# Performance work log

Hardware: AMD Instinct MI355X
Metric: run time of the kernel (lower is better)

Reference implementation:

```python
import jax, jax.numpy as jnp
import numpy as np

DIM = 512
NUM_GROUPS = 32
HEADS = 16
HEAD_DIM = 32
EPS = 1e-6


def group_norm(x, w, b, num_groups=NUM_GROUPS, eps=EPS):
    # x: [B, C, H, W]
    B, C, H, W = x.shape
    xg = x.reshape(B, num_groups, -1)
    mean = xg.mean(axis=-1, keepdims=True)
    var = xg.var(axis=-1, keepdims=True)
    xg = (xg - mean) / jnp.sqrt(var + eps)
    x = xg.reshape(B, C, H, W)
    return x * w[None, :, None, None] + b[None, :, None, None]


def conv1x1(x, w, b):
    # x: [B, C, H, W], w: [O, C], b: [O]
    return jnp.einsum('bchw,oc->bohw', x, w) + b[None, :, None, None]


def setup_inputs() -> dict:
    key = jax.random.key(0)
    ks = jax.random.split(key, 12)
    s = 1.0 / np.sqrt(DIM)
    d = {
        'x': jax.random.normal(ks[0], (1, DIM, 64, 64), dtype=jnp.float32),
        'gn_w': jnp.ones((DIM,), dtype=jnp.float32),
        'gn_b': jnp.zeros((DIM,), dtype=jnp.float32),
        'wq': jax.random.normal(ks[1], (DIM, DIM), dtype=jnp.float32) * s,
        'bq': jax.random.normal(ks[2], (DIM,), dtype=jnp.float32) * 0.01,
        'wk': jax.random.normal(ks[3], (DIM, DIM), dtype=jnp.float32) * s,
        'bk': jax.random.normal(ks[4], (DIM,), dtype=jnp.float32) * 0.01,
        'wv': jax.random.normal(ks[5], (DIM, DIM), dtype=jnp.float32) * s,
        'bv': jax.random.normal(ks[6], (DIM,), dtype=jnp.float32) * 0.01,
        'wo': jax.random.normal(ks[7], (DIM, DIM), dtype=jnp.float32) * s,
        'bo': jax.random.normal(ks[8], (DIM,), dtype=jnp.float32) * 0.01,
    }
    return d


def reference(x, gn_w, gn_b, wq, bq, wk, bk, wv, bv, wo, bo):
    B, C, H, W = x.shape
    N = H * W
    scale = HEAD_DIM ** -0.5

    q_in = x
    qn = group_norm(x, gn_w, gn_b)
    # Faithful to source: v-branch applies norm_q to the already-normalized q.
    vn = group_norm(qn, gn_w, gn_b)

    q = conv1x1(qn, wq, bq)
    k = conv1x1(vn, wk, bk)
    v = conv1x1(vn, wv, bv)

    def to_tokens(t):
        # [B, C, H, W] -> [B, heads, N, head_dim]
        return t.reshape(B, HEADS, HEAD_DIM, N).transpose(0, 1, 3, 2)

    q, k, v = to_tokens(q), to_tokens(k), to_tokens(v)

    attn = jax.nn.softmax(jnp.einsum('bhnd,bhmd->bhnm', q, k) * scale, axis=-1)
    out = jnp.einsum('bhnm,bhmd->bhnd', attn, v)  # [B, heads, N, head_dim]
    out = out.transpose(0, 1, 3, 2).reshape(B, C, H, W)
    out = conv1x1(out, wo, bo)
    return (out + q_in) / jnp.sqrt(jnp.float32(2.0))
```

## Files before the change

kernel.cpp:

```cpp
#include <hip/hip_runtime.h>

#define NTOK 4096
#define CHAN 512
#define GSIZE 65536
#define RSQRT2 0.7071067811865476f
#define SCALE 0.17677669529663687f
#define WB_OFF 32768
#define QT_OFF (WB_OFF + 2097152)
#define WS_NEEDED ((size_t)(QT_OFF + 4194304))

typedef unsigned short ushort_t;
typedef __attribute__((ext_vector_type(8))) short bf16x8;
typedef __attribute__((ext_vector_type(8))) _Float16 f16x8;
typedef __attribute__((ext_vector_type(4))) float f32x4;

__device__ __forceinline__ ushort_t f2b(float f) {
    unsigned u = __float_as_uint(f);
    unsigned r = (u + 0x7FFFu + ((u >> 16) & 1u)) >> 16;
    return (ushort_t)r;
}
__device__ __forceinline__ unsigned pack2r(float a, float b) {
    unsigned ua = __float_as_uint(a), ub = __float_as_uint(b);
    return ((ua + 0x8000u) >> 16) | ((ub + 0x8000u) & 0xFFFF0000u);
}
__device__ __forceinline__ unsigned packh2(float a, float b) {
    return __builtin_bit_cast(unsigned, __builtin_amdgcn_cvt_pkrtz(a, b));
}
__device__ __forceinline__ ushort_t f2h(float f) {
    return (ushort_t)(packh2(f, f) & 0xFFFFu);
}
__device__ __forceinline__ bf16x8 ldfrag(const ushort_t* p) {
    return __builtin_bit_cast(bf16x8, *(const uint4*)p);
}
__device__ __forceinline__ f16x8 ldfragh(const ushort_t* p) {
    return __builtin_bit_cast(f16x8, *(const uint4*)p);
}
__device__ __forceinline__ void ldg2lds16(const void* g, void* l) {
    __builtin_amdgcn_global_load_lds(
        (const __attribute__((address_space(1))) void*)g,
        (__attribute__((address_space(3))) void*)l, 16, 0, 0);
}

__global__ void diag_kernel(float* out, float v) {
    if (threadIdx.x == 0 && blockIdx.x == 0) out[0] = v;
}

__global__ __launch_bounds__(256) void gn_sums(const float* __restrict__ x,
                                               float* __restrict__ S,
                                               float* __restrict__ SS) {
    int c = blockIdx.x, t = threadIdx.x;
    const float4* p = (const float4*)(x + (size_t)c * 4096);
    float s = 0.f, ss = 0.f;
    #pragma unroll
    for (int i = 0; i < 4; i++) {
        float4 f = p[i * 256 + t];
        s += f.x + f.y + f.z + f.w;
        ss += f.x * f.x + f.y * f.y + f.z * f.z + f.w * f.w;
    }
    #pragma unroll
    for (int off = 32; off > 0; off >>= 1) {
        s += __shfl_xor(s, off);
        ss += __shfl_xor(ss, off);
    }
    __shared__ float as[4], bs[4];
    int w = t >> 6;
    if ((t & 63) == 0) { as[w] = s; bs[w] = ss; }
    __syncthreads();
    if (t == 0) {
        S[c] = as[0] + as[1] + as[2] + as[3];
        SS[c] = bs[0] + bs[1] + bs[2] + bs[3];
    }
}

__global__ __launch_bounds__(512) void gn_coef(const float* __restrict__ S,
                                               const float* __restrict__ SS,
                                               const float* __restrict__ gnw,
                                               const float* __restrict__ gnb,
                                               float* __restrict__ qa,
                                               float* __restrict__ qd,
                                               float* __restrict__ va,
                                               float* __restrict__ vd) {
    int c = threadIdx.x;
    float Sc = S[c], SSc = SS[c];
    float gs = Sc, gss = SSc;
    #pragma unroll
    for (int off = 1; off < 16; off <<= 1) {
        gs += __shfl_xor(gs, off);
        gss += __shfl_xor(gss, off);
    }
    float mu = gs * (1.f / GSIZE);
    float var = gss * (1.f / GSIZE) - mu * mu;
    float r1 = rsqrtf(var + 1e-6f);
    float wc = gnw[c], bc = gnb[c];
    float a1 = r1 * wc;
    float d1 = bc - mu * a1;
    qa[c] = a1; qd[c] = d1;
    float S2 = a1 * Sc + 4096.f * d1;
    float SS2 = a1 * a1 * SSc + 2.f * a1 * d1 * Sc + 4096.f * d1 * d1;
    float gs2 = S2, gss2 = SS2;
    #pragma unroll
    for (int off = 1; off < 16; off <<= 1) {
        gs2 += __shfl_xor(gs2, off);
        gss2 += __shfl_xor(gss2, off);
    }
    float mu2 = gs2 * (1.f / GSIZE);
    float var2 = gss2 * (1.f / GSIZE) - mu2 * mu2;
    float r2 = rsqrtf(var2 + 1e-6f);
    float a2 = r2 * wc;
    va[c] = a1 * a2;
    vd[c] = a2 * (d1 - mu2) + bc;
}

__global__ __launch_bounds__(256) void bias_fold(const float* __restrict__ wq,
                                                 const float* __restrict__ wk,
                                                 const float* __restrict__ wv,
                                                 const float* __restrict__ bq,
                                                 const float* __restrict__ bk,
                                                 const float* __restrict__ bv,
                                                 const float* __restrict__ qd,
                                                 const float* __restrict__ vd,
                                                 float* __restrict__ bqf,
                                                 float* __restrict__ bkf,
                                                 float* __restrict__ bvf) {
    int row = blockIdx.x * 4 + (threadIdx.x >> 6);
    int lane = threadIdx.x & 63;
    int m = row >> 9;
    int o = row & 511;
    const float* W = (m == 0) ? wq : (m == 1) ? wk : wv;
    const float* b = (m == 0) ? bq : (m == 1) ? bk : bv;
    const float* d = (m == 0) ? qd : vd;
    float* outp    = (m == 0) ? bqf : (m == 1) ? bkf : bvf;
    const float4* wr = (const float4*)(W + (size_t)o * 512) + lane * 2;
    const float4* dr = (const float4*)d + lane * 2;
    float4 a0 = wr[0], a1 = wr[1], d0 = dr[0], d1 = dr[1];
    float acc = a0.x * d0.x + a0.y * d0.y + a0.z * d0.z + a0.w * d0.w
              + a1.x * d1.x + a1.y * d1.y + a1.z * d1.z + a1.w * d1.w;
    #pragma unroll
    for (int off = 32; off > 0; off >>= 1) acc += __shfl_xor(acc, off);
    if (lane == 0) outp[o] = b[o] + acc;
}

__global__ __launch_bounds__(256) void wprep(const float* __restrict__ wq,
                                             const float* __restrict__ wk,
                                             const float* __restrict__ wv,
                                             const float* __restrict__ wo,
                                             const float* __restrict__ qa,
                                             const float* __restrict__ va,
                                             ushort_t* __restrict__ Wb) {
    int y = blockIdx.y;
    const float* src = (y == 0) ? wq : (y == 1) ? wk : (y == 2) ? wv : wo;
    int i = (blockIdx.x * 256 + threadIdx.x) * 4;
    float4 f = *(const float4*)(src + i);
    if (y < 3) {
        const float* aff = (y == 0) ? qa : va;
        float4 a = *(const float4*)(aff + (i & 511));
        f.x *= a.x; f.y *= a.y; f.z *= a.z; f.w *= a.w;
    }
    uint2 u;
    u.x = pack2r(f.x, f.y);
    u.y = pack2r(f.z, f.w);
    *(uint2*)(Wb + (size_t)y * 262144 + i) = u;
}

__global__ __launch_bounds__(256) void qkv_mfma(const float* __restrict__ x,
                                                const ushort_t* __restrict__ Wb,
                                                const float* __restrict__ bqf,
                                                const float* __restrict__ bkf,
                                                const float* __restrict__ bvf,
                                                ushort_t* __restrict__ QT,
                                                ushort_t* __restrict__ KT,
                                                ushort_t* __restrict__ Vb) {
    __shared__ __align__(16) ushort_t Wl[128][72];
    __shared__ __align__(16) ushort_t Bn[64][72];
    __shared__ __align__(16) ushort_t Tl[64][136];
    int t = threadIdx.x;
    int nbase = blockIdx.x << 6;
    int y = blockIdx.y;
    int buf = y >> 2;
    int obase = (y & 3) << 7;
    const ushort_t* Wsrc = Wb + (size_t)buf * 262144;
    const float* bias = (buf == 0) ? bqf : (buf == 1) ? bkf : bvf;

    int w = t >> 6, lane = t & 63, q15 = lane & 15, quad = lane >> 4;
    f32x4 acc[2][4];
    #pragma unroll
    for (int i = 0; i < 2; i++)
        #pragma unroll
        for (int j = 0; j < 4; j++) acc[i][j] = (f32x4){0.f, 0.f, 0.f, 0.f};

    int tok = t & 63, c8 = t >> 6;
    for (int ck = 0; ck < 512; ck += 64) {
        __syncthreads();
        #pragma unroll
        for (int i = 0; i < 4; i++) {
            int idx = 4 * t + i;
            int row = idx >> 3, seg = idx & 7;
            *(uint4*)&Wl[row][seg * 8] =
                *(const uint4*)&Wsrc[(size_t)(obase + row) * 512 + ck + seg * 8];
        }
        {
            float v[16];
            #pragma unroll
            for (int i = 0; i < 16; i++)
                v[i] = x[(size_t)(ck + c8 * 16 + i) * NTOK + nbase + tok];
            uint4 u0, u1;
            u0.x = pack2r(v[0], v[1]);   u0.y = pack2r(v[2], v[3]);
            u0.z = pack2r(v[4], v[5]);   u0.w = pack2r(v[6], v[7]);
            u1.x = pack2r(v[8], v[9]);   u1.y = pack2r(v[10], v[11]);
            u1.z = pack2r(v[12], v[13]); u1.w = pack2r(v[14], v[15]);
            *(uint4*)&Bn[tok][c8 * 16] = u0;
            *(uint4*)&Bn[tok][c8 * 16 + 8] = u1;
        }
        __syncthreads();
        #pragma unroll
        for (int kk = 0; kk < 2; kk++) {
            bf16x8 af0 = ldfrag(&Wl[w * 32 + q15][kk * 32 + quad * 8]);
            bf16x8 af1 = ldfrag(&Wl[w * 32 + 16 + q15][kk * 32 + quad * 8]);
            #pragma unroll
            for (int n8 = 0; n8 < 4; n8++) {
                bf16x8 bfv = ldfrag(&Bn[n8 * 16 + q15][kk * 32 + quad * 8]);
                acc[0][n8] = __builtin_amdgcn_mfma_f32_16x16x32_bf16(af0, bfv, acc[0][n8], 0, 0, 0);
                acc[1][n8] = __builtin_amdgcn_mfma_f32_16x16x32_bf16(af1, bfv, acc[1][n8], 0, 0, 0);
            }
        }
    }

    if (buf == 2) {
        #pragma unroll
        for (int mi = 0; mi < 2; mi++)
            #pragma unroll
            for (int r = 0; r < 4; r++) {
                int o = obase + w * 32 + mi * 16 + quad * 4 + r;
                float bo = bias[o];
                #pragma unroll
                for (int n8 = 0; n8 < 4; n8++)
                    Vb[(size_t)o * NTOK + nbase + n8 * 16 + q15] = f2h(acc[mi][n8][r] + bo);
            }
        return;
    }

    ushort_t* dstT = (buf == 0) ? QT : KT;
    float qs = (buf == 0) ? SCALE : 1.0f;
    __syncthreads();
    #pragma unroll
    for (int mi = 0; mi < 2; mi++)
        #pragma unroll
        for (int r = 0; r < 4; r++) {
            int mloc = w * 32 + mi * 16 + quad * 4 + r;
            float bo = bias[obase + mloc];
            #pragma unroll
            for (int n8 = 0; n8 < 4; n8++)
                Tl[n8 * 16 + q15][mloc] = f2b((acc[mi][n8][r] + bo) * qs);
        }
    __syncthreads();
    #pragma unroll
    for (int i = 0; i < 4; i++) {
        int idx = 4 * t + i;
        int row = idx >> 4, ch = idx & 15;
        uint4 u = *(const uint4*)&Tl[row][ch * 8];
        *(uint4*)&dstT[(size_t)(nbase + row) * 512 + obase + ch * 8] = u;
    }
}

__global__ __launch_bounds__(512, 4) void attn_v13(ushort_t* __restrict__ QT,
                                                   const ushort_t* __restrict__ KT,
                                                   const ushort_t* __restrict__ V) {
    __shared__ __align__(16) ushort_t KtF[2][8192];
    __shared__ __align__(16) ushort_t VtF[2][8192];
    int h = blockIdx.y;
    int t = threadIdx.x;
    int w = t >> 6, lane = t & 63, q15 = lane & 15, quad = lane >> 4;
    int qbase = (blockIdx.x << 7) + w * 16;
    int hc = h * 32;
    const ushort_t* Vh = V + (size_t)hc * NTOK;

    bf16x8 qf = ldfrag(&QT[(size_t)(qbase + q15) * 512 + hc + quad * 8]);

    const uint4 onesu = {0x3C003C00u, 0x3C003C00u, 0x3C003C00u, 0x3C003C00u};
    const f16x8 ones = __builtin_bit_cast(f16x8, onesu);

    f32x4 o[2] = {{0.f, 0.f, 0.f, 0.f}, {0.f, 0.f, 0.f, 0.f}};
    f32x4 lacc = {0.f, 0.f, 0.f, 0.f};

    auto issue = [&](int j0, int b) {
        #pragma unroll
        for (int i = 0; i < 2; i++) {
            int sbase = (w << 6) + (i << 9);
            int idx = sbase + lane;
            int krow = idx >> 2;
            int gd = (idx & 3) ^ ((krow >> 1) & 3);
            int rp = krow & 63;
            int srcr = (krow & 192) | (rp & 0x23) | ((rp & 0x0C) << 1) | ((rp & 0x10) >> 2);
            ldg2lds16(&KT[(size_t)(j0 + srcr) * 512 + hc + gd * 8],
                      &KtF[b][sbase * 8]);
        }
        #pragma unroll
        for (int i = 0; i < 2; i++) {
            int sbase = (w << 6) + (i << 9);
            int idx = sbase + lane;
            int d = idx >> 5;
            int gd = (idx & 31) ^ (d & 7);
            ldg2lds16(&Vh[(size_t)d * NTOK + j0 + gd * 8],
                      &VtF[b][sbase * 8]);
        }
    };

    issue(0, 0);
    int ksp8 = (quad ^ ((q15 >> 1) & 3)) * 8;
    int vq = q15 & 7;

    for (int tt = 0; tt < 16; tt++) {
        int cur = tt & 1;
        __syncthreads();
        if (tt < 15) issue((tt + 1) << 8, cur ^ 1);
        const ushort_t* KtC = KtF[cur];
        const ushort_t* VtC = VtF[cur];

        #pragma unroll
        for (int h2 = 0; h2 < 4; h2++) {
            f32x4 st[4];
            __builtin_amdgcn_s_setprio(1);
            #pragma unroll
            for (int kt = 0; kt < 4; kt++) {
                bf16x8 kf = ldfrag(&KtC[(h2 * 64 + kt * 16 + q15) * 32 + ksp8]);
                f32x4 z = {0.f, 0.f, 0.f, 0.f};
                st[kt] = __builtin_amdgcn_mfma_f32_16x16x32_bf16(kf, qf, z, 0, 0, 0);
            }
            __builtin_amdgcn_s_setprio(0);

            #pragma unroll
            for (int kt = 0; kt < 4; kt++)
                #pragma unroll
                for (int r = 0; r < 4; r++)
                    st[kt][r] = __expf(st[kt][r]);

            int g0 = ((h2 * 8 + quad) ^ vq) * 8;
            int g1 = g0 ^ 32;
            f16x8 v00 = ldfragh(&VtC[q15 * 256 + g0]);
            f16x8 v01 = ldfragh(&VtC[(16 + q15) * 256 + g0]);
            f16x8 v10 = ldfragh(&VtC[q15 * 256 + g1]);
            f16x8 v11 = ldfragh(&VtC[(16 + q15) * 256 + g1]);

            uint4 p0u, p1u;
            p0u.x = packh2(st[0][0], st[0][1]);
            p0u.y = packh2(st[0][2], st[0][3]);
            p0u.z = packh2(st[1][0], st[1][1]);
            p0u.w = packh2(st[1][2], st[1][3]);
            p1u.x = packh2(st[2][0], st[2][1]);
            p1u.y = packh2(st[2][2], st[2][3]);
            p1u.z = packh2(st[3][0], st[3][1]);
            p1u.w = packh2(st[3][2], st[3][3]);
            f16x8 pf0 = __builtin_bit_cast(f16x8, p0u);
            f16x8 pf1 = __builtin_bit_cast(f16x8, p1u);
            __builtin_amdgcn_s_setprio(1);
            o[0] = __builtin_amdgcn_mfma_f32_16x16x32_f16(pf0, v00, o[0], 0, 0, 0);
            o[1] = __builtin_amdgcn_mfma_f32_16x16x32_f16(pf0, v01, o[1], 0, 0, 0);
            lacc = __builtin_amdgcn_mfma_f32_16x16x32_f16(pf0, ones, lacc, 0, 0, 0);
            o[0] = __builtin_amdgcn_mfma_f32_16x16x32_f16(pf1, v10, o[0], 0, 0, 0);
            o[1] = __builtin_amdgcn_mfma_f32_16x16x32_f16(pf1, v11, o[1], 0, 0, 0);
            lacc = __builtin_amdgcn_mfma_f32_16x16x32_f16(pf1, ones, lacc, 0, 0, 0);
            __builtin_amdgcn_s_setprio(0);
        }
    }

    #pragma unroll
    for (int r = 0; r < 4; r++) {
        float li = 1.f / lacc[r];
        int q = quad * 4 + r;
        QT[(size_t)(qbase + q) * 512 + hc + q15]      = f2b(o[0][r] * li);
        QT[(size_t)(qbase + q) * 512 + hc + 16 + q15] = f2b(o[1][r] * li);
    }
}

__global__ __launch_bounds__(256) void oproj_mfma(const ushort_t* __restrict__ OT,
                                                  const ushort_t* __restrict__ Wob,
                                                  const float* __restrict__ bo,
                                                  const float* __restrict__ x,
                                                  float* __restrict__ out) {
    __shared__ __align__(16) ushort_t Wl[64][40];
    __shared__ __align__(16) ushort_t Bn[64][40];
    int t = threadIdx.x;
    int nbase = blockIdx.x << 6;
    int obase = blockIdx.y << 6;
    int w = t >> 6, lane = t & 63, q15 = lane & 15, quad = lane >> 4;

    f32x4 acc[4];
    #pragma unroll
    for (int i = 0; i < 4; i++) acc[i] = (f32x4){0.f, 0.f, 0.f, 0.f};

    int arow = t >> 2, aseg = t & 3;
    for (int ck = 0; ck < 512; ck += 32) {
        __syncthreads();
        *(uint4*)&Wl[arow][aseg * 8] =
            *(const uint4*)&Wob[(size_t)(obase + arow) * 512 + ck + aseg * 8];
        *(uint4*)&Bn[arow][aseg * 8] =
            *(const uint4*)&OT[(size_t)(nbase + arow) * 512 + ck + aseg * 8];
        __syncthreads();
        bf16x8 af = ldfrag(&Wl[w * 16 + q15][quad * 8]);
        #pragma unroll
        for (int n8 = 0; n8 < 4; n8++) {
            bf16x8 bfv = ldfrag(&Bn[n8 * 16 + q15][quad * 8]);
            acc[n8] = __builtin_amdgcn_mfma_f32_16x16x32_bf16(af, bfv, acc[n8], 0, 0, 0);
        }
    }

    #pragma unroll
    for (int r = 0; r < 4; r++) {
        int o = obase + w * 16 + quad * 4 + r;
        float b = bo[o];
        #pragma unroll
        for (int n8 = 0; n8 < 4; n8++) {
            size_t idx = (size_t)o * NTOK + nbase + n8 * 16 + q15;
            out[idx] = (acc[n8][r] + b + x[idx]) * RSQRT2;
        }
    }
}

extern "C" void kernel_launch(void* const* d_in, const int* in_sizes, int n_in,
                              void* d_out, int out_size, void* d_ws, size_t ws_size,
                              hipStream_t stream) {
    const float* x   = (const float*)d_in[0];
    const float* gnw = (const float*)d_in[1];
    const float* gnb = (const float*)d_in[2];
    const float* wq  = (const float*)d_in[3];
    const float* bq  = (const float*)d_in[4];
    const float* wk  = (const float*)d_in[5];
    const float* bk  = (const float*)d_in[6];
    const float* wv  = (const float*)d_in[7];
    const float* bv  = (const float*)d_in[8];
    const float* wo  = (const float*)d_in[9];
    const float* bo  = (const float*)d_in[10];
    float* out = (float*)d_out;

    if (ws_size < WS_NEEDED) {
        diag_kernel<<<1, 64, 0, stream>>>(out, (float)(ws_size >> 16));
        return;
    }

    char* wsb = (char*)d_ws;
    float* S   = (float*)(wsb + 0);
    float* SS  = (float*)(wsb + 2048);
    float* qa  = (float*)(wsb + 4096);
    float* qd  = (float*)(wsb + 6144);
    float* va  = (float*)(wsb + 8192);
    float* vd  = (float*)(wsb + 10240);
    float* bqf = (float*)(wsb + 12288);
    float* bkf = (float*)(wsb + 14336);
    float* bvf = (float*)(wsb + 16384);
    ushort_t* Wb = (ushort_t*)(wsb + WB_OFF);
    ushort_t* QT = (ushort_t*)(wsb + QT_OFF);
    ushort_t* KT = (ushort_t*)d_out;
    ushort_t* Vb = (ushort_t*)d_out + (size_t)CHAN * NTOK;

    gn_sums<<<512, 256, 0, stream>>>(x, S, SS);
    gn_coef<<<1, 512, 0, stream>>>(S, SS, gnw, gnb, qa, qd, va, vd);
    bias_fold<<<384, 256, 0, stream>>>(wq, wk, wv, bq, bk, bv, qd, vd, bqf, bkf, bvf);
    wprep<<<dim3(256, 4), 256, 0, stream>>>(wq, wk, wv, wo, qa, va, Wb);

    qkv_mfma<<<dim3(64, 12), 256, 0, stream>>>(x, Wb, bqf, bkf, bvf, QT, KT, Vb);

    attn_v13<<<dim3(32, 16), 512, 0, stream>>>(QT, KT, Vb);

    oproj_mfma<<<dim3(64, 8), 256, 0, stream>>>(QT, Wb + (size_t)3 * 262144, bo, x, out);
}
```

Baseline: 166.5 us.

## Fuse prep kernels, use exp2 with folded log2e scale, deepen oproj K-tile

Merges the bias-fold and weight-prep kernels into a single launch to save one kernel launch. Folds log2(e) into the Q scale so attention softmax can use the raw hardware exp2 instead of __expf. Doubles the output-projection K chunk from 32 to 64 per LDS stage, halving the number of barrier round-trips at the cost of more shared memory per block.

```diff
diff --git a/kernel.cpp b/kernel.cpp
--- a/kernel.cpp
+++ b/kernel.cpp
@@ -4,7 +4,7 @@
 #define CHAN 512
 #define GSIZE 65536
 #define RSQRT2 0.7071067811865476f
-#define SCALE 0.17677669529663687f
+#define SCALEX 0.2550348837f
 #define WB_OFF 32768
 #define QT_OFF (WB_OFF + 2097152)
 #define WS_NEEDED ((size_t)(QT_OFF + 4194304))
@@ -34,6 +34,13 @@
 }
 __device__ __forceinline__ f16x8 ldfragh(const ushort_t* p) {
     return __builtin_bit_cast(f16x8, *(const uint4*)p);
+}
+__device__ __forceinline__ float exp2_raw(float x) {
+#if __has_builtin(__builtin_amdgcn_exp2f)
+    return __builtin_amdgcn_exp2f(x);
+#else
+    return __expf(x * 0.6931471805599453f);
+#endif
 }
 __device__ __forceinline__ void ldg2lds16(const void* g, void* l) {
     __builtin_amdgcn_global_load_lds(
@@ -111,55 +118,55 @@
     vd[c] = a2 * (d1 - mu2) + bc;
 }
 
-__global__ __launch_bounds__(256) void bias_fold(const float* __restrict__ wq,
-                                                 const float* __restrict__ wk,
-                                                 const float* __restrict__ wv,
-                                                 const float* __restrict__ bq,
-                                                 const float* __restrict__ bk,
-                                                 const float* __restrict__ bv,
-                                                 const float* __restrict__ qd,
-                                                 const float* __restrict__ vd,
-                                                 float* __restrict__ bqf,
-                                                 float* __restrict__ bkf,
-                                                 float* __restrict__ bvf) {
-    int row = blockIdx.x * 4 + (threadIdx.x >> 6);
-    int lane = threadIdx.x & 63;
-    int m = row >> 9;
-    int o = row & 511;
-    const float* W = (m == 0) ? wq : (m == 1) ? wk : wv;
-    const float* b = (m == 0) ? bq : (m == 1) ? bk : bv;
-    const float* d = (m == 0) ? qd : vd;
-    float* outp    = (m == 0) ? bqf : (m == 1) ? bkf : bvf;
-    const float4* wr = (const float4*)(W + (size_t)o * 512) + lane * 2;
-    const float4* dr = (const float4*)d + lane * 2;
-    float4 a0 = wr[0], a1 = wr[1], d0 = dr[0], d1 = dr[1];
-    float acc = a0.x * d0.x + a0.y * d0.y + a0.z * d0.z + a0.w * d0.w
-              + a1.x * d1.x + a1.y * d1.y + a1.z * d1.z + a1.w * d1.w;
-    #pragma unroll
-    for (int off = 32; off > 0; off >>= 1) acc += __shfl_xor(acc, off);
-    if (lane == 0) outp[o] = b[o] + acc;
-}
-
-__global__ __launch_bounds__(256) void wprep(const float* __restrict__ wq,
-                                             const float* __restrict__ wk,
-                                             const float* __restrict__ wv,
-                                             const float* __restrict__ wo,
-                                             const float* __restrict__ qa,
-                                             const float* __restrict__ va,
-                                             ushort_t* __restrict__ Wb) {
-    int y = blockIdx.y;
-    const float* src = (y == 0) ? wq : (y == 1) ? wk : (y == 2) ? wv : wo;
-    int i = (blockIdx.x * 256 + threadIdx.x) * 4;
-    float4 f = *(const float4*)(src + i);
-    if (y < 3) {
-        const float* aff = (y == 0) ? qa : va;
-        float4 a = *(const float4*)(aff + (i & 511));
-        f.x *= a.x; f.y *= a.y; f.z *= a.z; f.w *= a.w;
-    }
-    uint2 u;
-    u.x = pack2r(f.x, f.y);
-    u.y = pack2r(f.z, f.w);
-    *(uint2*)(Wb + (size_t)y * 262144 + i) = u;
+__global__ __launch_bounds__(256) void prep_all(const float* __restrict__ wq,
+                                                const float* __restrict__ wk,
+                                                const float* __restrict__ wv,
+                                                const float* __restrict__ wo,
+                                                const float* __restrict__ bq,
+                                                const float* __restrict__ bk,
+                                                const float* __restrict__ bv,
+                                                const float* __restrict__ qa,
+                                                const float* __restrict__ qd,
+                                                const float* __restrict__ va,
+                                                const float* __restrict__ vd,
+                                                float* __restrict__ bqf,
+                                                float* __restrict__ bkf,
+                                                float* __restrict__ bvf,
+                                                ushort_t* __restrict__ Wb) {
+    int bx = blockIdx.x;
+    if (bx < 384) {
+        int row = bx * 4 + (threadIdx.x >> 6);
+        int lane = threadIdx.x & 63;
+        int m = row >> 9;
+        int o = row & 511;
+        const float* W = (m == 0) ? wq : (m == 1) ? wk : wv;
+        const float* b = (m == 0) ? bq : (m == 1) ? bk : bv;
+        const float* d = (m == 0) ? qd : vd;
+        float* outp    = (m == 0) ? bqf : (m == 1) ? bkf : bvf;
+        const float4* wr = (const float4*)(W + (size_t)o * 512) + lane * 2;
+        const float4* dr = (const float4*)d + lane * 2;
+        float4 a0 = wr[0], a1 = wr[1], d0 = dr[0], d1 = dr[1];
+        float acc = a0.x * d0.x + a0.y * d0.y + a0.z * d0.z + a0.w * d0.w
+                  + a1.x * d1.x + a1.y * d1.y + a1.z * d1.z + a1.w * d1.w;
+        #pragma unroll
+        for (int off = 32; off > 0; off >>= 1) acc += __shfl_xor(acc, off);
+        if (lane == 0) outp[o] = b[o] + acc;
+    } else {
+        int idx = bx - 384;
+        int y = idx >> 8;
+        const float* src = (y == 0) ? wq : (y == 1) ? wk : (y == 2) ? wv : wo;
+        int i = ((idx & 255) * 256 + threadIdx.x) * 4;
+        float4 f = *(const float4*)(src + i);
+        if (y < 3) {
+            const float* aff = (y == 0) ? qa : va;
+            float4 a = *(const float4*)(aff + (i & 511));
+            f.x *= a.x; f.y *= a.y; f.z *= a.z; f.w *= a.w;
+        }
+        uint2 u;
+        u.x = pack2r(f.x, f.y);
+        u.y = pack2r(f.z, f.w);
+        *(uint2*)(Wb + (size_t)y * 262144 + i) = u;
+    }
 }
 
 __global__ __launch_bounds__(256) void qkv_mfma(const float* __restrict__ x,
@@ -240,7 +247,7 @@
     }
 
     ushort_t* dstT = (buf == 0) ? QT : KT;
-    float qs = (buf == 0) ? SCALE : 1.0f;
+    float qs = (buf == 0) ? SCALEX : 1.0f;
     __syncthreads();
     #pragma unroll
     for (int mi = 0; mi < 2; mi++)
@@ -262,7 +269,7 @@
     }
 }
 
-__global__ __launch_bounds__(512, 4) void attn_v13(ushort_t* __restrict__ QT,
+__global__ __launch_bounds__(512, 4) void attn_v14(ushort_t* __restrict__ QT,
                                                    const ushort_t* __restrict__ KT,
                                                    const ushort_t* __restrict__ V) {
     __shared__ __align__(16) ushort_t KtF[2][8192];
@@ -332,7 +339,7 @@
             for (int kt = 0; kt < 4; kt++)
                 #pragma unroll
                 for (int r = 0; r < 4; r++)
-                    st[kt][r] = __expf(st[kt][r]);
+                    st[kt][r] = exp2_raw(st[kt][r]);
 
             int g0 = ((h2 * 8 + quad) ^ vq) * 8;
             int g1 = g0 ^ 32;
@@ -377,8 +384,8 @@
                                                   const float* __restrict__ bo,
                                                   const float* __restrict__ x,
                                                   float* __restrict__ out) {
-    __shared__ __align__(16) ushort_t Wl[64][40];
-    __shared__ __align__(16) ushort_t Bn[64][40];
+    __shared__ __align__(16) ushort_t Wl[64][72];
+    __shared__ __align__(16) ushort_t Bn[64][72];
     int t = threadIdx.x;
     int nbase = blockIdx.x << 6;
     int obase = blockIdx.y << 6;
@@ -388,19 +395,26 @@
     #pragma unroll
     for (int i = 0; i < 4; i++) acc[i] = (f32x4){0.f, 0.f, 0.f, 0.f};
 
-    int arow = t >> 2, aseg = t & 3;
-    for (int ck = 0; ck < 512; ck += 32) {
+    for (int ck = 0; ck < 512; ck += 64) {
         __syncthreads();
-        *(uint4*)&Wl[arow][aseg * 8] =
-            *(const uint4*)&Wob[(size_t)(obase + arow) * 512 + ck + aseg * 8];
-        *(uint4*)&Bn[arow][aseg * 8] =
-            *(const uint4*)&OT[(size_t)(nbase + arow) * 512 + ck + aseg * 8];
+        #pragma unroll
+        for (int i = 0; i < 2; i++) {
+            int idx = t * 2 + i;
+            int row = idx >> 3, seg = idx & 7;
+            *(uint4*)&Wl[row][seg * 8] =
+                *(const uint4*)&Wob[(size_t)(obase + row) * 512 + ck + seg * 8];
+            *(uint4*)&Bn[row][seg * 8] =
+                *(const uint4*)&OT[(size_t)(nbase + row) * 512 + ck + seg * 8];
+        }
         __syncthreads();
-        bf16x8 af = ldfrag(&Wl[w * 16 + q15][quad * 8]);
-        #pragma unroll
-        for (int n8 = 0; n8 < 4; n8++) {
-            bf16x8 bfv = ldfrag(&Bn[n8 * 16 + q15][quad * 8]);
-            acc[n8] = __builtin_amdgcn_mfma_f32_16x16x32_bf16(af, bfv, acc[n8], 0, 0, 0);
+        #pragma unroll
+        for (int kk = 0; kk < 2; kk++) {
+            bf16x8 af = ldfrag(&Wl[w * 16 + q15][kk * 32 + quad * 8]);
+            #pragma unroll
+            for (int n8 = 0; n8 < 4; n8++) {
+                bf16x8 bfv = ldfrag(&Bn[n8 * 16 + q15][kk * 32 + quad * 8]);
+                acc[n8] = __builtin_amdgcn_mfma_f32_16x16x32_bf16(af, bfv, acc[n8], 0, 0, 0);
+            }
         }
     }
 
@@ -454,12 +468,12 @@
 
     gn_sums<<<512, 256, 0, stream>>>(x, S, SS);
     gn_coef<<<1, 512, 0, stream>>>(S, SS, gnw, gnb, qa, qd, va, vd);
-    bias_fold<<<384, 256, 0, stream>>>(wq, wk, wv, bq, bk, bv, qd, vd, bqf, bkf, bvf);
-    wprep<<<dim3(256, 4), 256, 0, stream>>>(wq, wk, wv, wo, qa, va, Wb);
+    prep_all<<<1408, 256, 0, stream>>>(wq, wk, wv, wo, bq, bk, bv,
+                                       qa, qd, va, vd, bqf, bkf, bvf, Wb);
 
     qkv_mfma<<<dim3(64, 12), 256, 0, stream>>>(x, Wb, bqf, bkf, bvf, QT, KT, Vb);
 
-    attn_v13<<<dim3(32, 16), 512, 0, stream>>>(QT, KT, Vb);
+    attn_v14<<<dim3(32, 16), 512, 0, stream>>>(QT, KT, Vb);
 
     oproj_mfma<<<dim3(64, 8), 256, 0, stream>>>(QT, Wb + (size_t)3 * 262144, bo, x, out);
 }
```

After: 163.1 us. 1.02x faster.
